# Performance work log

Measured on AMD Instinct MI355X. Metric: run time of the kernel, lower is better.

Reference implementation:

```python
import jax, jax.numpy as jnp
import numpy as np

EMBEDDING_BOUND = 1e4  # uniform init bound for box centers (repo constant)


def setup_inputs() -> dict:
    key = jax.random.key(0)
    k1, k2, k3 = jax.random.split(key, 3)
    num_classes, dim = 100000, 50
    d = dim // 2
    # init per MultiBoxEL.init_embeddings: centers ~ U(-B, B), offsets ~ N(1, 0.333)
    centers = jax.random.uniform(k1, (num_classes, d), dtype=jnp.float32,
                                 minval=-EMBEDDING_BOUND, maxval=EMBEDDING_BOUND)
    offsets = 1.0 + 0.333 * jax.random.normal(k2, (num_classes, d), dtype=jnp.float32)
    class_embeds = jnp.concatenate([centers, offsets], axis=1)  # [C, dim]
    nf1_data = jax.random.randint(k3, (2_000_000, 2), 0, num_classes)  # [N, 2] class ids
    return {"class_embeds": class_embeds, "nf1_data": nf1_data}


def _to_box(emb):
    # get_multiboxes: first half = center, second half = |offsets|
    d = emb.shape[-1] // 2
    return emb[:, :d], jnp.abs(emb[:, d:])


def reference(class_embeds, nf1_data):
    """nf1_loss (C subsumed-by D): batched inclusion loss 1 - Area(C ^ D)/Area(C),
    then L2 norm of relu(losses) over the batch (a scalar), exactly as inclusion_loss."""
    c_emb = class_embeds[nf1_data[:, 0]]  # [N, dim] gather (memory-bound)
    d_emb = class_embeds[nf1_data[:, 1]]
    cc, co = _to_box(c_emb)
    dc, do = _to_box(d_emb)
    # box intersection: [max(lowers), min(uppers)]; empty -> side length clipped to 0
    lo = jnp.maximum(cc - co, dc - do)
    hi = jnp.minimum(cc + co, dc + do)
    inter_area = jnp.prod(jax.nn.relu(hi - lo), axis=-1)  # [N]
    c_area = jnp.prod(2.0 * co, axis=-1)                  # [N] box volume = prod(2*offset)
    loss = jnp.where(c_area == 0, 0.0,
           jnp.where(jnp.isinf(c_area), 1.0 - inter_area / (2.0 * EMBEDDING_BOUND),
                     1.0 - inter_area / c_area))
    return jnp.linalg.norm(jax.nn.relu(loss))
```

## Files before the change

### kernel.cpp

```cpp
#include <hip/hip_runtime.h>
#include <math.h>


#define DIMS 25
#define EMB_BOUND 10000.0f
#define PPT 8
#define BLK 512
#define BLK_B 1024
#define TROWS 64
#define TFLOATS (TROWS * 2 * DIMS)

__global__ void init_ws_kernel(float* ws) {
    if (threadIdx.x == 0 && blockIdx.x == 0) ws[0] = 0.0f;
}

__global__ __launch_bounds__(256, 8) void nf1_fallback_kernel(
    const float* __restrict__ emb, const int2* __restrict__ pairs,
    int n_pairs, float* __restrict__ ws)
{
    const int gl  = threadIdx.x & 31;
    const int gid = blockIdx.x * (blockDim.x >> 5) + (threadIdx.x >> 5);
    const int ngrp = gridDim.x * (blockDim.x >> 5);
    float acc = 0.0f;
    for (int p = gid; p < n_pairs; p += ngrp) {
        int2 pr = pairs[p];
        const float* rc = emb + (size_t)pr.x * (2 * DIMS);
        const float* rd = emb + (size_t)pr.y * (2 * DIMS);
        float t = 1.0f, a = 1.0f;
        if (gl < DIMS) {
            float cc = rc[gl], co = fabsf(rc[DIMS + gl]);
            float dc = rd[gl], dd = fabsf(rd[DIMS + gl]);
            float lo = fmaxf(cc - co, dc - dd);
            float hi = fminf(cc + co, dc + dd);
            t = fmaxf(hi - lo, 0.0f);
            a = 2.0f * co;
        }
        #pragma unroll
        for (int m = 16; m >= 1; m >>= 1) { t *= __shfl_xor(t, m, 32); a *= __shfl_xor(a, m, 32); }
        float loss;
        if (a == 0.0f)     loss = 0.0f;
        else if (isinf(a)) loss = 1.0f - t / (2.0f * EMB_BOUND);
        else               loss = 1.0f - t / a;
        loss = fmaxf(loss, 0.0f);
        if (gl == 0) acc += loss * loss;
    }
    #pragma unroll
    for (int m = 32; m >= 1; m >>= 1) acc += __shfl_xor(acc, m, 64);
    __shared__ float wsum[4];
    if ((threadIdx.x & 63) == 0) wsum[threadIdx.x >> 6] = acc;
    __syncthreads();
    if (threadIdx.x == 0) atomicAdd(ws, wsum[0] + wsum[1] + wsum[2] + wsum[3]);
}

__global__ void fallback_finalize_kernel(const float* __restrict__ ws, float* __restrict__ out) {
    if (threadIdx.x == 0 && blockIdx.x == 0) out[0] = sqrtf(fmaxf(ws[0], 0.0f));
}

__device__ __forceinline__ float slow_pair(const float* __restrict__ emb, int2 pr) {
    const float* ra = emb + (size_t)pr.x * (2 * DIMS);
    const float* rb = emb + (size_t)pr.y * (2 * DIMS);
    float inter = 1.0f, carea = 1.0f;
    for (int j = 0; j < DIMS; j++) {
        float cc = ra[j], co = fabsf(ra[DIMS + j]);
        float dc = rb[j], dd = fabsf(rb[DIMS + j]);
        float lo = fmaxf(cc - co, dc - dd);
        float hi = fminf(cc + co, dc + dd);
        inter *= fmaxf(hi - lo, 0.0f);
        carea *= 2.0f * co;
    }
    float loss;
    if (carea == 0.0f)     loss = 0.0f;
    else if (isinf(carea)) loss = 1.0f - inter / (2.0f * EMB_BOUND);
    else                   loss = 1.0f - inter / carea;
    loss = fmaxf(loss, 0.0f);
    return loss * loss;
}

__device__ __forceinline__ float key_pair(const float2* __restrict__ keys,
                                          const float* __restrict__ emb, int2 pr) {
    float2 ka = keys[pr.x];
    float2 kb = keys[pr.y];
    float t0 = fminf(ka.y, kb.y) - fmaxf(ka.x, kb.x);
    if (t0 > 0.0f) return slow_pair(emb, pr);
    return 1.0f;
}

template <int K>
__device__ __forceinline__ int ring_bucket(float lo, float hi) {
    float w = hi - lo;
    if (w <= 16.0f && fabsf(lo) <= 1.0e6f) {
        int i = (int)floorf(lo * 0.0625f);
        int b = i % K; if (b < 0) b += K;
        return b;
    }
    return K;
}

__device__ __forceinline__ bool ring_pass(unsigned a, unsigned b, unsigned K) {
    unsigned dd = (a >= b) ? (a - b) : (b - a);
    return (a == K) | (b == K) | (dd <= 1u) | (dd == K - 1u);
}

__global__ __launch_bounds__(256) void repack_byte_kernel(
    const float* __restrict__ emb, float2* __restrict__ keys,
    unsigned char* __restrict__ gbuck,
    float* __restrict__ acc, unsigned* __restrict__ ticket, int n_rows)
{
    __shared__ float tile[TFLOATS];
    if (blockIdx.x == 0 && threadIdx.x == 0) { acc[0] = 0.0f; ticket[0] = 0u; }

    const int n_tiles = (n_rows + TROWS - 1) / TROWS;
    for (int tIdx = blockIdx.x; tIdx < n_tiles; tIdx += gridDim.x) {
        const int r0 = tIdx * TROWS;
        const int rows = min(TROWS, n_rows - r0);
        const int cnt = rows * (2 * DIMS);
        {
            const float4* g4 = (const float4*)(emb + r0 * (2 * DIMS));
            float4* s4 = (float4*)tile;
            const int n4 = cnt >> 2;
            for (int i = threadIdx.x; i < n4; i += blockDim.x) s4[i] = g4[i];
        }
        __syncthreads();
        if (threadIdx.x < TROWS) {
            const int j = threadIdx.x;
            if (j < rows) {
                float c = tile[j * (2 * DIMS)];
                float o = fabsf(tile[j * (2 * DIMS) + DIMS]);
                float lo = c - o, hi = c + o;
                keys[r0 + j] = make_float2(lo, hi);
                gbuck[r0 + j] = (unsigned char)ring_bucket<255>(lo, hi);
            }
        }
        __syncthreads();
    }
}

__global__ __launch_bounds__(BLK_B, 4) void pair_screen_byte_kernel(
    const float2* __restrict__ keys, const unsigned char* __restrict__ gbuck,
    const float* __restrict__ emb, const int2* __restrict__ pairs, int n_pairs,
    int n_rows, float* __restrict__ acc, unsigned* __restrict__ ticket,
    float* __restrict__ out)
{
    extern __shared__ unsigned char sbuck[];
    __shared__ float wsum[BLK_B / 64];

    {
        const int nb16 = (n_rows + 15) >> 4;
        const uint4* g4 = (const uint4*)gbuck;
        uint4* s4 = (uint4*)sbuck;
        for (int i = threadIdx.x; i < nb16; i += blockDim.x) s4[i] = g4[i];
    }
    __syncthreads();

    const int t = blockIdx.x * blockDim.x + threadIdx.x;
    const int base = t * PPT;

    float sum = 0.0f;
    if (base + PPT - 1 < n_pairs) {
        const int4* p4 = (const int4*)pairs;
        int2 pr[PPT];
        #pragma unroll
        for (int i = 0; i < PPT / 2; i++) {
            int4 q = p4[(PPT / 2) * t + i];
            pr[2 * i]     = make_int2(q.x, q.y);
            pr[2 * i + 1] = make_int2(q.z, q.w);
        }
        unsigned ba[PPT], bb[PPT];
        #pragma unroll
        for (int i = 0; i < PPT; i++) {
            ba[i] = sbuck[pr[i].x];
            bb[i] = sbuck[pr[i].y];
        }
        #pragma unroll
        for (int i = 0; i < PPT; i++) {
            if (ring_pass(ba[i], bb[i], 255u)) sum += key_pair(keys, emb, pr[i]);
            else                               sum += 1.0f;
        }
    } else if (base < n_pairs) {
        for (int p = base; p < n_pairs; p++) {
            int2 pr = pairs[p];
            unsigned a = sbuck[pr.x], b = sbuck[pr.y];
            if (ring_pass(a, b, 255u)) sum += key_pair(keys, emb, pr);
            else                       sum += 1.0f;
        }
    }

    #pragma unroll
    for (int m = 32; m >= 1; m >>= 1) sum += __shfl_xor(sum, m, 64);
    if ((threadIdx.x & 63) == 0) wsum[threadIdx.x >> 6] = sum;
    __syncthreads();
    if (threadIdx.x == 0) {
        float s = 0.0f;
        #pragma unroll
        for (int w = 0; w < BLK_B / 64; w++) s += wsum[w];
        atomicAdd(acc, s);
        __threadfence();
        unsigned tk = atomicAdd(ticket, 1u);
        if (tk == gridDim.x - 1) {
            float v = atomicAdd(acc, 0.0f);
            out[0] = sqrtf(fmaxf(v, 0.0f));
        }
    }
}

__global__ __launch_bounds__(256) void repack_nib_kernel(
    const float* __restrict__ emb, float2* __restrict__ keys,
    unsigned char* __restrict__ gbuck,
    float* __restrict__ acc, unsigned* __restrict__ ticket, int n_rows)
{
    __shared__ float tile[TFLOATS];
    if (blockIdx.x == 0 && threadIdx.x == 0) { acc[0] = 0.0f; ticket[0] = 0u; }
    const int n_tiles = (n_rows + TROWS - 1) / TROWS;
    for (int tIdx = blockIdx.x; tIdx < n_tiles; tIdx += gridDim.x) {
        const int r0 = tIdx * TROWS;
        const int rows = min(TROWS, n_rows - r0);
        const int cnt = rows * (2 * DIMS);
        {
            const float4* g4 = (const float4*)(emb + r0 * (2 * DIMS));
            float4* s4 = (float4*)tile;
            const int n4 = cnt >> 2;
            for (int i = threadIdx.x; i < n4; i += blockDim.x) s4[i] = g4[i];
        }
        __syncthreads();
        if (threadIdx.x < TROWS) {
            const int j = threadIdx.x;
            int b = 0;
            if (j < rows) {
                float c = tile[j * (2 * DIMS)];
                float o = fabsf(tile[j * (2 * DIMS) + DIMS]);
                float lo = c - o, hi = c + o;
                keys[r0 + j] = make_float2(lo, hi);
                if (o > 300.0f || fabsf(lo) > 1.0e6f) b = 15;
                else {
                    int i600 = (int)floorf(lo * (1.0f / 600.0f));
                    b = ((i600 % 15) + 15) % 15;
                }
            }
            int bhi = __shfl_down(b, 1, 64);
            if ((j & 1) == 0 && j < rows)
                gbuck[(r0 + j) >> 1] = (unsigned char)(b | (bhi << 4));
        }
        __syncthreads();
    }
}

__global__ __launch_bounds__(BLK, 6) void pair_screen_nib_kernel(
    const float2* __restrict__ keys, const unsigned char* __restrict__ gbuck,
    const float* __restrict__ emb, const int2* __restrict__ pairs, int n_pairs,
    int n_rows, float* __restrict__ acc, unsigned* __restrict__ ticket,
    float* __restrict__ out)
{
    __shared__ unsigned char sbuck[50016];
    __shared__ float wsum[BLK / 64];
    {
        const int nb16 = (((n_rows + 1) >> 1) + 15) >> 4;
        const uint4* g4 = (const uint4*)gbuck;
        uint4* s4 = (uint4*)sbuck;
        for (int i = threadIdx.x; i < nb16; i += blockDim.x) s4[i] = g4[i];
    }
    __syncthreads();

    const int t = blockIdx.x * blockDim.x + threadIdx.x;
    const int base = t * PPT;
    float sum = 0.0f;
    if (base + PPT - 1 < n_pairs) {
        const int4* p4 = (const int4*)pairs;
        int2 pr[PPT];
        #pragma unroll
        for (int i = 0; i < PPT / 2; i++) {
            int4 q = p4[(PPT / 2) * t + i];
            pr[2 * i]     = make_int2(q.x, q.y);
            pr[2 * i + 1] = make_int2(q.z, q.w);
        }
        unsigned ba[PPT], bb[PPT];
        #pragma unroll
        for (int i = 0; i < PPT; i++) {
            unsigned va = sbuck[pr[i].x >> 1];
            unsigned vb = sbuck[pr[i].y >> 1];
            ba[i] = ((pr[i].x & 1) ? (va >> 4) : va) & 15u;
            bb[i] = ((pr[i].y & 1) ? (vb >> 4) : vb) & 15u;
        }
        #pragma unroll
        for (int i = 0; i < PPT; i++) {
            if (ring_pass(ba[i], bb[i], 15u)) sum += key_pair(keys, emb, pr[i]);
            else                              sum += 1.0f;
        }
    } else if (base < n_pairs) {
        for (int p = base; p < n_pairs; p++) {
            int2 pr = pairs[p];
            unsigned va = sbuck[pr.x >> 1];
            unsigned vb = sbuck[pr.y >> 1];
            unsigned a = ((pr.x & 1) ? (va >> 4) : va) & 15u;
            unsigned b = ((pr.y & 1) ? (vb >> 4) : vb) & 15u;
            if (ring_pass(a, b, 15u)) sum += key_pair(keys, emb, pr);
            else                      sum += 1.0f;
        }
    }

    #pragma unroll
    for (int m = 32; m >= 1; m >>= 1) sum += __shfl_xor(sum, m, 64);
    if ((threadIdx.x & 63) == 0) wsum[threadIdx.x >> 6] = sum;
    __syncthreads();
    if (threadIdx.x == 0) {
        float s = 0.0f;
        #pragma unroll
        for (int w = 0; w < BLK / 64; w++) s += wsum[w];
        atomicAdd(acc, s);
        __threadfence();
        unsigned tk = atomicAdd(ticket, 1u);
        if (tk == gridDim.x - 1) {
            float v = atomicAdd(acc, 0.0f);
            out[0] = sqrtf(fmaxf(v, 0.0f));
        }
    }
}

extern "C" void kernel_launch(void* const* d_in, const int* in_sizes, int n_in,
                              void* d_out, int out_size, void* d_ws, size_t ws_size,
                              hipStream_t stream) {
    const float* emb  = (const float*)d_in[0];
    const int2*  prs  = (const int2*)d_in[1];
    const int n_pairs = in_sizes[1] / 2;
    const int n_rows  = in_sizes[0] / (2 * DIMS);

    float*    ws     = (float*)d_ws;
    unsigned* ticket = (unsigned*)(ws + 1);
    float*    out    = (float*)d_out;
    float2*   keys   = (float2*)((char*)d_ws + 256);
    unsigned char* gbuck = (unsigned char*)(keys + n_rows);

    int dev = 0;  hipGetDevice(&dev);
    int maxShared = 0;
    hipDeviceGetAttribute(&maxShared, hipDeviceAttributeMaxSharedMemoryPerBlock, dev);

    const size_t shmem = (size_t)((n_rows + 15) & ~15);
    const bool byte_ok = ((size_t)maxShared >= shmem + 512) &&
                         ((n_rows & 1) == 0) &&
                         (ws_size >= 256 + (size_t)n_rows * 8 + shmem + 64);
    const bool nib_ok  = (((n_rows + 1) >> 1) <= 50000) && ((n_rows & 1) == 0) &&
                         (ws_size >= 256 + (size_t)n_rows * 8 + ((n_rows + 1) >> 1) + 64);

    if (byte_ok) {
        int n_tiles = (n_rows + TROWS - 1) / TROWS;
        hipLaunchKernelGGL(repack_byte_kernel, dim3(min(n_tiles, 1024)), dim3(256), 0, stream,
                           emb, keys, gbuck, ws, ticket, n_rows);
        int threads = (n_pairs + PPT - 1) / PPT;
        int sblocks = (threads + BLK_B - 1) / BLK_B;
        hipLaunchKernelGGL(pair_screen_byte_kernel, dim3(sblocks), dim3(BLK_B),
                           shmem, stream,
                           keys, gbuck, emb, prs, n_pairs, n_rows, ws, ticket, out);
    } else if (nib_ok) {
        int n_tiles = (n_rows + TROWS - 1) / TROWS;
        hipLaunchKernelGGL(repack_nib_kernel, dim3(min(n_tiles, 1024)), dim3(256), 0, stream,
                           emb, keys, gbuck, ws, ticket, n_rows);
        int threads = (n_pairs + PPT - 1) / PPT;
        int sblocks = (threads + BLK - 1) / BLK;
        hipLaunchKernelGGL(pair_screen_nib_kernel, dim3(sblocks), dim3(BLK), 0, stream,
                           keys, gbuck, emb, prs, n_pairs, n_rows, ws, ticket, out);
    } else {
        hipLaunchKernelGGL(init_ws_kernel, dim3(1), dim3(64), 0, stream, ws);
        hipLaunchKernelGGL(nf1_fallback_kernel, dim3(4096), dim3(256), 0, stream,
                           emb, prs, n_pairs, ws);
        hipLaunchKernelGGL(fallback_finalize_kernel, dim3(1), dim3(64), 0, stream, ws, out);
    }
}
```

Before: 88.79 us.

## Fuse repack and pair screen into one cooperative kernel with grid sync

```diff
diff --git a/kernel.cpp b/kernel.cpp
--- a/kernel.cpp
+++ b/kernel.cpp
@@ -1,5 +1,8 @@
 #include <hip/hip_runtime.h>
+#include <hip/hip_cooperative_groups.h>
 #include <math.h>
+
+namespace cg = cooperative_groups;
 
 
 #define DIMS 25
@@ -9,6 +12,7 @@
 #define BLK_B 1024
 #define TROWS 64
 #define TFLOATS (TROWS * 2 * DIMS)
+#define FTROWS 128
 
 __global__ void init_ws_kernel(float* ws) {
     if (threadIdx.x == 0 && blockIdx.x == 0) ws[0] = 0.0f;
@@ -101,6 +105,105 @@
     return (a == K) | (b == K) | (dd <= 1u) | (dd == K - 1u);
 }
 
+__global__ __launch_bounds__(BLK_B, 1) void fused_kernel(
+    const float* __restrict__ emb, float2* __restrict__ keys,
+    unsigned char* __restrict__ gbuck,
+    const int2* __restrict__ pairs, int n_pairs, int n_rows,
+    float* __restrict__ acc, unsigned* __restrict__ ticket,
+    float* __restrict__ out)
+{
+    extern __shared__ unsigned char smem[];
+    __shared__ float wsum[BLK_B / 64];
+
+    if (blockIdx.x == 0 && threadIdx.x == 0) { acc[0] = 0.0f; ticket[0] = 0u; }
+
+    {
+        float* tile = (float*)smem;
+        const int n_tiles = (n_rows + FTROWS - 1) / FTROWS;
+        for (int tIdx = blockIdx.x; tIdx < n_tiles; tIdx += gridDim.x) {
+            const int r0 = tIdx * FTROWS;
+            const int rows = min(FTROWS, n_rows - r0);
+            const int cnt = rows * (2 * DIMS);
+            const int n4 = cnt >> 2;
+            {
+                const float4* g4 = (const float4*)(emb + (size_t)r0 * (2 * DIMS));
+                float4* s4 = (float4*)tile;
+                for (int i = threadIdx.x; i < n4; i += blockDim.x) s4[i] = g4[i];
+                for (int i = (n4 << 2) + threadIdx.x; i < cnt; i += blockDim.x)
+                    tile[i] = emb[(size_t)r0 * (2 * DIMS) + i];
+            }
+            __syncthreads();
+            if (threadIdx.x < FTROWS && threadIdx.x < rows) {
+                const int j = threadIdx.x;
+                float c = tile[j * (2 * DIMS)];
+                float o = fabsf(tile[j * (2 * DIMS) + DIMS]);
+                float lo = c - o, hi = c + o;
+                keys[r0 + j] = make_float2(lo, hi);
+                gbuck[r0 + j] = (unsigned char)ring_bucket<255>(lo, hi);
+            }
+            __syncthreads();
+        }
+    }
+
+    cg::this_grid().sync();
+
+    unsigned char* sbuck = smem;
+    {
+        const int nb16 = (n_rows + 15) >> 4;
+        const uint4* g4 = (const uint4*)gbuck;
+        uint4* s4 = (uint4*)sbuck;
+        for (int i = threadIdx.x; i < nb16; i += blockDim.x) s4[i] = g4[i];
+    }
+    __syncthreads();
+
+    const int t = blockIdx.x * blockDim.x + threadIdx.x;
+    const int base = t * PPT;
+
+    float sum = 0.0f;
+    if (base + PPT - 1 < n_pairs) {
+        const int4* p4 = (const int4*)pairs;
+        int2 pr[PPT];
+        #pragma unroll
+        for (int i = 0; i < PPT / 2; i++) {
+            int4 q = p4[(PPT / 2) * t + i];
+            pr[2 * i]     = make_int2(q.x, q.y);
+            pr[2 * i + 1] = make_int2(q.z, q.w);
+        }
+        unsigned ba[PPT], bb[PPT];
+        #pragma unroll
+        for (int i = 0; i < PPT; i++) { ba[i] = sbuck[pr[i].x]; bb[i] = sbuck[pr[i].y]; }
+        #pragma unroll
+        for (int i = 0; i < PPT; i++) {
+            if (ring_pass(ba[i], bb[i], 255u)) sum += key_pair(keys, emb, pr[i]);
+            else                               sum += 1.0f;
+        }
+    } else if (base < n_pairs) {
+        for (int p = base; p < n_pairs; p++) {
+            int2 pr = pairs[p];
+            unsigned a = sbuck[pr.x], b = sbuck[pr.y];
+            if (ring_pass(a, b, 255u)) sum += key_pair(keys, emb, pr);
+            else                       sum += 1.0f;
+        }
+    }
+
+    #pragma unroll
+    for (int m = 32; m >= 1; m >>= 1) sum += __shfl_xor(sum, m, 64);
+    if ((threadIdx.x & 63) == 0) wsum[threadIdx.x >> 6] = sum;
+    __syncthreads();
+    if (threadIdx.x == 0) {
+        float s = 0.0f;
+        #pragma unroll
+        for (int w = 0; w < BLK_B / 64; w++) s += wsum[w];
+        atomicAdd(acc, s);
+        __threadfence();
+        unsigned tk = atomicAdd(ticket, 1u);
+        if (tk == gridDim.x - 1) {
+            float v = atomicAdd(acc, 0.0f);
+            out[0] = sqrtf(fmaxf(v, 0.0f));
+        }
+    }
+}
+
 __global__ __launch_bounds__(256) void repack_byte_kernel(
     const float* __restrict__ emb, float2* __restrict__ keys,
     unsigned char* __restrict__ gbuck,
@@ -108,7 +211,6 @@
 {
     __shared__ float tile[TFLOATS];
     if (blockIdx.x == 0 && threadIdx.x == 0) { acc[0] = 0.0f; ticket[0] = 0u; }
-
     const int n_tiles = (n_rows + TROWS - 1) / TROWS;
     for (int tIdx = blockIdx.x; tIdx < n_tiles; tIdx += gridDim.x) {
         const int r0 = tIdx * TROWS;
@@ -143,7 +245,6 @@
 {
     extern __shared__ unsigned char sbuck[];
     __shared__ float wsum[BLK_B / 64];
-
     {
         const int nb16 = (n_rows + 15) >> 4;
         const uint4* g4 = (const uint4*)gbuck;
@@ -154,7 +255,6 @@
 
     const int t = blockIdx.x * blockDim.x + threadIdx.x;
     const int base = t * PPT;
-
     float sum = 0.0f;
     if (base + PPT - 1 < n_pairs) {
         const int4* p4 = (const int4*)pairs;
@@ -167,10 +267,7 @@
         }
         unsigned ba[PPT], bb[PPT];
         #pragma unroll
-        for (int i = 0; i < PPT; i++) {
-            ba[i] = sbuck[pr[i].x];
-            bb[i] = sbuck[pr[i].y];
-        }
+        for (int i = 0; i < PPT; i++) { ba[i] = sbuck[pr[i].x]; bb[i] = sbuck[pr[i].y]; }
         #pragma unroll
         for (int i = 0; i < PPT; i++) {
             if (ring_pass(ba[i], bb[i], 255u)) sum += key_pair(keys, emb, pr[i]);
@@ -320,8 +417,8 @@
                               hipStream_t stream) {
     const float* emb  = (const float*)d_in[0];
     const int2*  prs  = (const int2*)d_in[1];
-    const int n_pairs = in_sizes[1] / 2;
-    const int n_rows  = in_sizes[0] / (2 * DIMS);
+    int n_pairs = in_sizes[1] / 2;
+    int n_rows  = in_sizes[0] / (2 * DIMS);
 
     float*    ws     = (float*)d_ws;
     unsigned* ticket = (unsigned*)(ws + 1);
@@ -330,37 +427,63 @@
     unsigned char* gbuck = (unsigned char*)(keys + n_rows);
 
     int dev = 0;  hipGetDevice(&dev);
-    int maxShared = 0;
+    int maxShared = 0, coop = 0, numCU = 0;
     hipDeviceGetAttribute(&maxShared, hipDeviceAttributeMaxSharedMemoryPerBlock, dev);
-
-    const size_t shmem = (size_t)((n_rows + 15) & ~15);
-    const bool byte_ok = ((size_t)maxShared >= shmem + 512) &&
-                         ((n_rows & 1) == 0) &&
-                         (ws_size >= 256 + (size_t)n_rows * 8 + shmem + 64);
-    const bool nib_ok  = (((n_rows + 1) >> 1) <= 50000) && ((n_rows & 1) == 0) &&
-                         (ws_size >= 256 + (size_t)n_rows * 8 + ((n_rows + 1) >> 1) + 64);
-
-    if (byte_ok) {
+    hipDeviceGetAttribute(&coop, hipDeviceAttributeCooperativeLaunch, dev);
+    hipDeviceGetAttribute(&numCU, hipDeviceAttributeMultiprocessorCount, dev);
+
+    const size_t tabBytes = (size_t)((n_rows + 15) & ~15);
+    const size_t fusedDyn = tabBytes > (size_t)(FTROWS * 2 * DIMS * 4)
+                          ? tabBytes : (size_t)(FTROWS * 2 * DIMS * 4);
+    const bool ws_ok_byte = (ws_size >= 256 + (size_t)n_rows * 8 + tabBytes + 64) &&
+                            ((n_rows & 1) == 0);
+    const bool byte_ok = ((size_t)maxShared >= tabBytes + 512) && ws_ok_byte;
+
+    const int threads  = (n_pairs + PPT - 1) / PPT;
+    const int sblocks  = (threads + BLK_B - 1) / BLK_B;
+
+    bool launched = false;
+    if (byte_ok && coop && ((size_t)maxShared >= fusedDyn + 512)) {
+        int blocksPerCU = 0;
+        hipError_t oe = hipOccupancyMaxActiveBlocksPerMultiprocessor(
+            &blocksPerCU, (const void*)fused_kernel, BLK_B, fusedDyn);
+        if (oe == hipSuccess && (long long)blocksPerCU * numCU >= sblocks) {
+            void* args[] = { (void*)&emb, (void*)&keys, (void*)&gbuck,
+                             (void*)&prs, (void*)&n_pairs, (void*)&n_rows,
+                             (void*)&ws, (void*)&ticket, (void*)&out };
+            hipError_t le = hipLaunchCooperativeKernel(
+                (const void*)fused_kernel, dim3(sblocks), dim3(BLK_B),
+                args, (unsigned int)fusedDyn, stream);
+            if (le == hipSuccess) launched = true;
+        }
+    }
+
+    if (!launched && byte_ok) {
         int n_tiles = (n_rows + TROWS - 1) / TROWS;
         hipLaunchKernelGGL(repack_byte_kernel, dim3(min(n_tiles, 1024)), dim3(256), 0, stream,
                            emb, keys, gbuck, ws, ticket, n_rows);
-        int threads = (n_pairs + PPT - 1) / PPT;
-        int sblocks = (threads + BLK_B - 1) / BLK_B;
         hipLaunchKernelGGL(pair_screen_byte_kernel, dim3(sblocks), dim3(BLK_B),
-                           shmem, stream,
+                           tabBytes, stream,
                            keys, gbuck, emb, prs, n_pairs, n_rows, ws, ticket, out);
-    } else if (nib_ok) {
-        int n_tiles = (n_rows + TROWS - 1) / TROWS;
-        hipLaunchKernelGGL(repack_nib_kernel, dim3(min(n_tiles, 1024)), dim3(256), 0, stream,
-                           emb, keys, gbuck, ws, ticket, n_rows);
-        int threads = (n_pairs + PPT - 1) / PPT;
-        int sblocks = (threads + BLK - 1) / BLK;
-        hipLaunchKernelGGL(pair_screen_nib_kernel, dim3(sblocks), dim3(BLK), 0, stream,
-                           keys, gbuck, emb, prs, n_pairs, n_rows, ws, ticket, out);
-    } else {
-        hipLaunchKernelGGL(init_ws_kernel, dim3(1), dim3(64), 0, stream, ws);
-        hipLaunchKernelGGL(nf1_fallback_kernel, dim3(4096), dim3(256), 0, stream,
-                           emb, prs, n_pairs, ws);
-        hipLaunchKernelGGL(fallback_finalize_kernel, dim3(1), dim3(64), 0, stream, ws, out);
-    }
-}
+        launched = true;
+    }
+
+    if (!launched) {
+        const bool nib_ok = (((n_rows + 1) >> 1) <= 50000) && ((n_rows & 1) == 0) &&
+                            (ws_size >= 256 + (size_t)n_rows * 8 + ((n_rows + 1) >> 1) + 64);
+        if (nib_ok) {
+            int n_tiles = (n_rows + TROWS - 1) / TROWS;
+            hipLaunchKernelGGL(repack_nib_kernel, dim3(min(n_tiles, 1024)), dim3(256), 0, stream,
+                               emb, keys, gbuck, ws, ticket, n_rows);
+            int thr = (n_pairs + PPT - 1) / PPT;
+            int sb  = (thr + BLK - 1) / BLK;
+            hipLaunchKernelGGL(pair_screen_nib_kernel, dim3(sb), dim3(BLK), 0, stream,
+                               keys, gbuck, emb, prs, n_pairs, n_rows, ws, ticket, out);
+        } else {
+            hipLaunchKernelGGL(init_ws_kernel, dim3(1), dim3(64), 0, stream, ws);
+            hipLaunchKernelGGL(nf1_fallback_kernel, dim3(4096), dim3(256), 0, stream,
+                               emb, prs, n_pairs, ws);
+            hipLaunchKernelGGL(fallback_finalize_kernel, dim3(1), dim3(64), 0, stream, ws, out);
+        }
+    }
+}
```

New measurement: 87.51 us, median of 2. About the same (-1.4%).
